# Kernel tuning notes

Hardware: AMD Instinct MI355X
Metric: run time of the kernel (lower is better)

## Reference

```python
import jax, jax.numpy as jnp
import numpy as np

ALPHA = 1.702   # GLU sigmoid scale
LIMIT = 7.0     # clamp limit
K = 2           # experts per token


def setup_inputs() -> dict:
    key = jax.random.key(0)
    ks = jax.random.split(key, 4)
    B, S, H, E, I = 1, 1024, 1024, 8, 1024
    return {
        "hidden_states": jax.random.normal(ks[0], (B, S, H), jnp.float32),
        "router_weight": jax.random.normal(ks[1], (E, H), jnp.float32),
        "router_bias": jnp.zeros((E,), jnp.float32),
        "gate_up_proj": jax.random.normal(ks[2], (E, H, 2 * I), jnp.float32) * 0.02,
        "gate_up_bias": jnp.zeros((E, 2 * I), jnp.float32),
        "down_proj": jax.random.normal(ks[3], (E, I, H), jnp.float32) * 0.02,
        "down_bias": jnp.zeros((E, H), jnp.float32),
    }


def reference(hidden_states, router_weight, router_bias, gate_up_proj,
              gate_up_bias, down_proj, down_bias):
    B, S, H = hidden_states.shape
    E = router_weight.shape[0]
    I = down_proj.shape[1]
    T = B * S

    flat = hidden_states.reshape(T, H)

    # Router: softmax over experts, top-K selection (weights NOT renormalized).
    logits = flat @ router_weight.T + router_bias               # [T, E]
    scores = jax.nn.softmax(logits, axis=-1)
    topk_vals, topk_idx = jax.lax.top_k(scores, K)              # [T, K]

    # Dense per-token expert weight matrix (equivalent of dispatch metadata +
    # combine * topk_weights in the tt pipeline); top-k indices are unique.
    w = jnp.zeros((T, E), scores.dtype).at[
        jnp.arange(T)[:, None], topk_idx].set(topk_vals)        # [T, E]

    # Expert MLP with clamped GLU (gpt-oss style).
    gu = jnp.einsum('th,ehf->tef', flat, gate_up_proj) + gate_up_bias  # [T,E,2I]
    gate = jnp.minimum(gu[..., :I], LIMIT)
    up = jnp.clip(gu[..., I:], -LIMIT, LIMIT)
    glu = gate * jax.nn.sigmoid(gate * ALPHA)
    act = (up + 1.0) * glu                                       # [T, E, I]

    down = jnp.einsum('tei,eih->teh', act, down_proj) + down_bias  # [T, E, H]

    # Weighted combine over selected experts.
    out = jnp.einsum('teh,te->th', down, w)
    return out.reshape(B, S, H)
```

## Files before the change

### kernel.cpp

```cpp
#include <hip/hip_runtime.h>
#include <hip/hip_bf16.h>


typedef unsigned short u16;
typedef __attribute__((ext_vector_type(8))) __bf16 bf16x8;
typedef __attribute__((ext_vector_type(4))) float f32x4;

#define T_TOK 1024
#define H_DIM 1024
#define E_NUM 8
#define I_DIM 1024
#define ALPHA 1.702f
#define LIMIT 7.0f
#define LSTR 72

__device__ __forceinline__ u16 f2bf(float f) {
    unsigned u = __builtin_bit_cast(unsigned, f);
    u = (u + 0x7FFFu + ((u >> 16) & 1u)) >> 16;
    return (u16)u;
}

__device__ __forceinline__ unsigned pk2(float lo, float hi) {
#if defined(__has_builtin) && __has_builtin(__builtin_amdgcn_cvt_pk_bf16_f32)
    typedef __attribute__((ext_vector_type(2))) __bf16 bf16x2_t;
    bf16x2_t v = __builtin_amdgcn_cvt_pk_bf16_f32(lo, hi);
    return __builtin_bit_cast(unsigned, v);
#else
    return (unsigned)f2bf(lo) | ((unsigned)f2bf(hi) << 16);
#endif
}

__device__ __forceinline__ f32x4 mfma16(bf16x8 a, bf16x8 b, f32x4 c) {
    return __builtin_amdgcn_mfma_f32_16x16x32_bf16(a, b, c, 0, 0, 0);
}

__device__ __forceinline__ void expert_range(const int* counts, int e,
                                             int& cnt, int& abase) {
    int a = 0, c = 0;
#pragma unroll
    for (int i = 0; i < E_NUM; ++i) {
        int v = counts[i];
        if (i < e) a += v;
        if (i == e) c = v;
    }
    cnt = c; abase = a;
}

__global__ void k_zero(int* counts) {
    if (threadIdx.x < E_NUM) counts[threadIdx.x] = 0;
}

__global__ __launch_bounds__(256) void k_router(
    const float* __restrict__ x, const float* __restrict__ rw,
    const float* __restrict__ rb, const float* __restrict__ db,
    int* __restrict__ counts, int* __restrict__ tok_list,
    float* __restrict__ w_list, u16* __restrict__ xb,
    float* __restrict__ out)
{
    const int t = blockIdx.x;
    const int tid = threadIdx.x;
    const float4 xv = *(const float4*)(x + (size_t)t * H_DIM + tid * 4);

    *(uint2*)(xb + (size_t)t * H_DIM + tid * 4) =
        make_uint2(pk2(xv.x, xv.y), pk2(xv.z, xv.w));

    float p[E_NUM];
#pragma unroll
    for (int e = 0; e < E_NUM; ++e) {
        const float4 wv = *(const float4*)(rw + e * H_DIM + tid * 4);
        p[e] = xv.x * wv.x + xv.y * wv.y + xv.z * wv.z + xv.w * wv.w;
    }
#pragma unroll
    for (int off = 32; off; off >>= 1) {
#pragma unroll
        for (int e = 0; e < E_NUM; ++e) p[e] += __shfl_down(p[e], off, 64);
    }
    __shared__ float red[4][E_NUM];
    __shared__ int se[2];
    __shared__ float sw[2];
    const int lane = tid & 63, wvid = tid >> 6;
    if (lane == 0) {
#pragma unroll
        for (int e = 0; e < E_NUM; ++e) red[wvid][e] = p[e];
    }
    __syncthreads();
    if (tid == 0) {
        float lg[E_NUM];
#pragma unroll
        for (int e = 0; e < E_NUM; ++e)
            lg[e] = red[0][e] + red[1][e] + red[2][e] + red[3][e] + rb[e];
        float m1 = -1e30f, m2 = -1e30f; int i1 = 0, i2 = 0;
#pragma unroll
        for (int e = 0; e < E_NUM; ++e) {
            float l = lg[e];
            if (l > m1) { m2 = m1; i2 = i1; m1 = l; i1 = e; }
            else if (l > m2) { m2 = l; i2 = e; }
        }
        float s = 0.f;
#pragma unroll
        for (int e = 0; e < E_NUM; ++e) s += __expf(lg[e] - m1);
        const float w0 = 1.0f / s;
        const float w1 = __expf(m2 - m1) / s;
        int slot0 = atomicAdd(&counts[i1], 1);
        tok_list[i1 * T_TOK + slot0] = t;
        w_list[i1 * T_TOK + slot0] = w0;
        int slot1 = atomicAdd(&counts[i2], 1);
        tok_list[i2 * T_TOK + slot1] = t;
        w_list[i2 * T_TOK + slot1] = w1;
        se[0] = i1; se[1] = i2; sw[0] = w0; sw[1] = w1;
    }
    __syncthreads();
    const int e0 = se[0], e1 = se[1];
    const float w0 = sw[0], w1 = sw[1];
    const int c = tid * 4;
    float4 d0 = *(const float4*)(db + e0 * H_DIM + c);
    float4 d1 = *(const float4*)(db + e1 * H_DIM + c);
    float4 o;
    o.x = w0 * d0.x + w1 * d1.x;
    o.y = w0 * d0.y + w1 * d1.y;
    o.z = w0 * d0.z + w1 * d1.z;
    o.w = w0 * d0.w + w1 * d1.w;
    *(float4*)(out + (size_t)t * H_DIM + c) = o;
}

__global__ __launch_bounds__(256) void k_gateup(
    const float* __restrict__ gup, const float* __restrict__ gub,
    const int* __restrict__ counts, const int* __restrict__ tok_list,
    const u16* __restrict__ xb, u16* __restrict__ act)
{
    const int e = blockIdx.z;
    int cnt, abase;
    expert_range(counts, e, cnt, abase);
    const int m0 = blockIdx.y * 64;
    if (m0 >= cnt) return;
    const int n0 = blockIdx.x * 32;
    const int tid = threadIdx.x;

    __shared__ __align__(16) u16 As[64 * LSTR];
    __shared__ __align__(16) u16 Bs[64 * LSTR];
    unsigned* Bs32 = (unsigned*)Bs;

    const int arow_i = tid >> 2, akq = (tid & 3) * 16;
    const int aslot = m0 + arow_i;
    const int atok = (aslot < cnt) ? tok_list[e * T_TOK + aslot] : 0;
    const u16* asrc = xb + (size_t)atok * H_DIM + akq;
    u16* adst = &As[arow_i * LSTR + akq];

    const int kp = tid >> 3, q = tid & 7;
    const float* bgate = gup + ((size_t)e << 21) + n0 + q * 4;

    const int lane = tid & 63, wv = tid >> 6;
    const int fm = lane & 15, kg = lane >> 4;

    f32x4 accg[2], accu[2];
#pragma unroll
    for (int nt = 0; nt < 2; ++nt) {
        accg[nt] = (f32x4){0.f, 0.f, 0.f, 0.f};
        accu[nt] = (f32x4){0.f, 0.f, 0.f, 0.f};
    }

#define GU_LOAD(A0, A1, G0, G1, U0, U1, KB)                                    \
    {                                                                          \
        const u16* ap_ = asrc + (KB);                                          \
        A0 = *(const uint4*)(ap_);                                             \
        A1 = *(const uint4*)(ap_ + 8);                                         \
        const float* gp_ = bgate + (size_t)((KB) + 2 * kp) * 2048;             \
        G0 = *(const float4*)(gp_);                                            \
        G1 = *(const float4*)(gp_ + 2048);                                     \
        U0 = *(const float4*)(gp_ + 1024);                                     \
        U1 = *(const float4*)(gp_ + 3072);                                     \
    }
#define GU_STORE(A0, A1, G0, G1, U0, U1)                                       \
    {                                                                          \
        *(uint4*)adst       = A0;                                              \
        *(uint4*)(adst + 8) = A1;                                              \
        const float* g0_ = (const float*)&G0; const float* g1_ = (const float*)&G1; \
        const float* u0_ = (const float*)&U0; const float* u1_ = (const float*)&U1; \
        _Pragma("unroll")                                                      \
        for (int j = 0; j < 4; ++j) {                                          \
            Bs32[(q * 4 + j) * 36 + kp]        = pk2(g0_[j], g1_[j]);          \
            Bs32[(32 + q * 4 + j) * 36 + kp]   = pk2(u0_[j], u1_[j]);          \
        }                                                                      \
    }
#define GU_MFMA()                                                              \
    {                                                                          \
        _Pragma("unroll")                                                      \
        for (int sub = 0; sub < 2; ++sub) {                                    \
            bf16x8 af = *(const bf16x8*)&As[(wv * 16 + fm) * LSTR + sub * 32 + kg * 8]; \
            _Pragma("unroll")                                                  \
            for (int nt = 0; nt < 2; ++nt) {                                   \
                bf16x8 bg = *(const bf16x8*)&Bs[(nt * 16 + fm) * LSTR + sub * 32 + kg * 8]; \
                bf16x8 bu = *(const bf16x8*)&Bs[(32 + nt * 16 + fm) * LSTR + sub * 32 + kg * 8]; \
                accg[nt] = mfma16(af, bg, accg[nt]);                           \
                accu[nt] = mfma16(af, bu, accu[nt]);                           \
            }                                                                  \
        }                                                                      \
    }

    uint4 a0s0, a1s0, a0s1, a1s1;
    float4 g0s0, g1s0, u0s0, u1s0, g0s1, g1s1, u0s1, u1s1;
    GU_LOAD(a0s0, a1s0, g0s0, g1s0, u0s0, u1s0, 0);
    GU_LOAD(a0s1, a1s1, g0s1, g1s1, u0s1, u1s1, 64);

    for (int kb = 0; kb < H_DIM; kb += 128) {
        __syncthreads();
        GU_STORE(a0s0, a1s0, g0s0, g1s0, u0s0, u1s0);
        if (kb + 128 < H_DIM) GU_LOAD(a0s0, a1s0, g0s0, g1s0, u0s0, u1s0, kb + 128);
        __syncthreads();
        GU_MFMA();

        __syncthreads();
        GU_STORE(a0s1, a1s1, g0s1, g1s1, u0s1, u1s1);
        if (kb + 192 < H_DIM) GU_LOAD(a0s1, a1s1, g0s1, g1s1, u0s1, u1s1, kb + 192);
        __syncthreads();
        GU_MFMA();
    }
#undef GU_LOAD
#undef GU_STORE
#undef GU_MFMA

#pragma unroll
    for (int r = 0; r < 4; ++r) {
        int rowb = wv * 16 + kg * 4 + r;
        int slot = m0 + rowb;
        if (slot >= cnt) continue;
        size_t arow_o = (size_t)(abase + slot) * I_DIM;
#pragma unroll
        for (int nt = 0; nt < 2; ++nt) {
            int cn = n0 + nt * 16 + fm;
            float g = accg[nt][r] + gub[e * 2048 + cn];
            float u = accu[nt][r] + gub[e * 2048 + 1024 + cn];
            g = fminf(g, LIMIT);
            u = fminf(fmaxf(u, -LIMIT), LIMIT);
            float glu = g / (1.f + __expf(-ALPHA * g));
            act[arow_o + cn] = f2bf((u + 1.f) * glu);
        }
    }
}

__global__ __launch_bounds__(256) void k_down(
    const float* __restrict__ dp,
    const int* __restrict__ counts, const int* __restrict__ tok_list,
    const float* __restrict__ w_list,
    const u16* __restrict__ act, float* __restrict__ out)
{
    const int e = blockIdx.z & 7, ks = blockIdx.z >> 3;
    int cnt, abase;
    expert_range(counts, e, cnt, abase);
    const int m0 = blockIdx.y * 64;
    if (m0 >= cnt) return;
    const int n0 = blockIdx.x * 64;
    const int tid = threadIdx.x;

    __shared__ __align__(16) u16 As[64 * LSTR];
    __shared__ __align__(16) u16 Bs[64 * LSTR];
    unsigned* Bs32 = (unsigned*)Bs;

    const int arow_i = tid >> 2, akq = (tid & 3) * 16;
    const u16* asrc = act + (size_t)(abase + m0 + arow_i) * I_DIM + ks * 512 + akq;
    u16* adst = &As[arow_i * LSTR + akq];

    const int kp = tid >> 3, q = tid & 7;
    const float* bsrc = dp + ((size_t)e << 20) + (size_t)(ks * 512) * 1024 + n0 + q * 4;

    const int lane = tid & 63, wv = tid >> 6;
    const int fm = lane & 15, kg = lane >> 4;

    f32x4 acc[4];
#pragma unroll
    for (int nt = 0; nt < 4; ++nt) acc[nt] = (f32x4){0.f, 0.f, 0.f, 0.f};

#define DN_LOAD(A0, A1, B00, B01, B10, B11, KB)                                \
    {                                                                          \
        const u16* ap_ = asrc + (KB);                                          \
        A0 = *(const uint4*)(ap_);                                             \
        A1 = *(const uint4*)(ap_ + 8);                                         \
        const float* bp_ = bsrc + (size_t)((KB) + 2 * kp) * 1024;              \
        B00 = *(const float4*)(bp_);                                           \
        B01 = *(const float4*)(bp_ + 1024);                                    \
        B10 = *(const float4*)(bp_ + 32);                                      \
        B11 = *(const float4*)(bp_ + 1056);                                    \
    }
#define DN_STORE(A0, A1, B00, B01, B10, B11)                                   \
    {                                                                          \
        *(uint4*)adst       = A0;                                              \
        *(uint4*)(adst + 8) = A1;                                              \
        const float* b00_ = (const float*)&B00; const float* b01_ = (const float*)&B01; \
        const float* b10_ = (const float*)&B10; const float* b11_ = (const float*)&B11; \
        _Pragma("unroll")                                                      \
        for (int j = 0; j < 4; ++j) {                                          \
            Bs32[(q * 4 + j) * 36 + kp]      = pk2(b00_[j], b01_[j]);          \
            Bs32[(32 + q * 4 + j) * 36 + kp] = pk2(b10_[j], b11_[j]);          \
        }                                                                      \
    }
#define DN_MFMA()                                                              \
    {                                                                          \
        _Pragma("unroll")                                                      \
        for (int sub = 0; sub < 2; ++sub) {                                    \
            bf16x8 af = *(const bf16x8*)&As[(wv * 16 + fm) * LSTR + sub * 32 + kg * 8]; \
            _Pragma("unroll")                                                  \
            for (int nt = 0; nt < 4; ++nt) {                                   \
                bf16x8 b = *(const bf16x8*)&Bs[(nt * 16 + fm) * LSTR + sub * 32 + kg * 8]; \
                acc[nt] = mfma16(af, b, acc[nt]);                              \
            }                                                                  \
        }                                                                      \
    }

    uint4 a0s0, a1s0, a0s1, a1s1;
    float4 b00s0, b01s0, b10s0, b11s0, b00s1, b01s1, b10s1, b11s1;
    DN_LOAD(a0s0, a1s0, b00s0, b01s0, b10s0, b11s0, 0);
    DN_LOAD(a0s1, a1s1, b00s1, b01s1, b10s1, b11s1, 64);

    for (int kb = 0; kb < 512; kb += 128) {
        __syncthreads();
        DN_STORE(a0s0, a1s0, b00s0, b01s0, b10s0, b11s0);
        if (kb + 128 < 512) DN_LOAD(a0s0, a1s0, b00s0, b01s0, b10s0, b11s0, kb + 128);
        __syncthreads();
        DN_MFMA();

        __syncthreads();
        DN_STORE(a0s1, a1s1, b00s1, b01s1, b10s1, b11s1);
        if (kb + 192 < 512) DN_LOAD(a0s1, a1s1, b00s1, b01s1, b10s1, b11s1, kb + 192);
        __syncthreads();
        DN_MFMA();
    }
#undef DN_LOAD
#undef DN_STORE
#undef DN_MFMA

#pragma unroll
    for (int r = 0; r < 4; ++r) {
        int rowb = wv * 16 + kg * 4 + r;
        int slot = m0 + rowb;
        if (slot >= cnt) continue;
        float wgt = w_list[e * T_TOK + slot];
        int tok = tok_list[e * T_TOK + slot];
        float* orow = out + (size_t)tok * H_DIM + n0;
#pragma unroll
        for (int nt = 0; nt < 4; ++nt)
            atomicAdd(orow + nt * 16 + fm, acc[nt][r] * wgt);
    }
}

extern "C" void kernel_launch(void* const* d_in, const int* in_sizes, int n_in,
                              void* d_out, int out_size, void* d_ws, size_t ws_size,
                              hipStream_t stream) {
    const float* x   = (const float*)d_in[0];
    const float* rw  = (const float*)d_in[1];
    const float* rb  = (const float*)d_in[2];
    const float* gup = (const float*)d_in[3];
    const float* gub = (const float*)d_in[4];
    const float* dp  = (const float*)d_in[5];
    const float* db  = (const float*)d_in[6];
    float* out = (float*)d_out;

    char* ws = (char*)d_ws;
    int*   counts   = (int*)(ws);
    int*   tok_list = (int*)(ws + 64);
    float* w_list   = (float*)(ws + 64 + 32768);
    u16*   xb       = (u16*)(ws + 65600);
    u16*   act      = (u16*)(ws + 65600 + 2097152);

    k_zero<<<1, 64, 0, stream>>>(counts);
    k_router<<<T_TOK, 256, 0, stream>>>(x, rw, rb, db, counts, tok_list, w_list,
                                        xb, out);
    k_gateup<<<dim3(32, 16, 8), 256, 0, stream>>>(gup, gub, counts, tok_list,
                                                  xb, act);
    k_down<<<dim3(16, 16, 16), 256, 0, stream>>>(dp, counts, tok_list, w_list,
                                                 act, out);
}
```

Before: 210.8 us.

## Double-buffer LDS tiles in gate-up and down expert GEMMs

Both expert GEMM kernels now keep two shared-memory A/B tile buffers. The next tile is written into one buffer while MFMAs read the other, which halves the barriers per k-step from four to two. Launch bounds also request four blocks per CU, trading register budget for occupancy. Shared memory per block doubles, which may limit residency or force register spills.

```diff
diff --git a/kernel.cpp b/kernel.cpp
--- a/kernel.cpp
+++ b/kernel.cpp
@@ -123,7 +123,7 @@
     *(float4*)(out + (size_t)t * H_DIM + c) = o;
 }
 
-__global__ __launch_bounds__(256) void k_gateup(
+__global__ __launch_bounds__(256, 4) void k_gateup(
     const float* __restrict__ gup, const float* __restrict__ gub,
     const int* __restrict__ counts, const int* __restrict__ tok_list,
     const u16* __restrict__ xb, u16* __restrict__ act)
@@ -136,15 +136,19 @@
     const int n0 = blockIdx.x * 32;
     const int tid = threadIdx.x;
 
-    __shared__ __align__(16) u16 As[64 * LSTR];
-    __shared__ __align__(16) u16 Bs[64 * LSTR];
-    unsigned* Bs32 = (unsigned*)Bs;
+    __shared__ __align__(16) u16 As0[64 * LSTR];
+    __shared__ __align__(16) u16 Bs0[64 * LSTR];
+    __shared__ __align__(16) u16 As1[64 * LSTR];
+    __shared__ __align__(16) u16 Bs1[64 * LSTR];
+    unsigned* B32_0 = (unsigned*)Bs0;
+    unsigned* B32_1 = (unsigned*)Bs1;
 
     const int arow_i = tid >> 2, akq = (tid & 3) * 16;
     const int aslot = m0 + arow_i;
     const int atok = (aslot < cnt) ? tok_list[e * T_TOK + aslot] : 0;
     const u16* asrc = xb + (size_t)atok * H_DIM + akq;
-    u16* adst = &As[arow_i * LSTR + akq];
+    u16* adst0 = &As0[arow_i * LSTR + akq];
+    u16* adst1 = &As1[arow_i * LSTR + akq];
 
     const int kp = tid >> 3, q = tid & 7;
     const float* bgate = gup + ((size_t)e << 21) + n0 + q * 4;
@@ -170,27 +174,27 @@
         U0 = *(const float4*)(gp_ + 1024);                                     \
         U1 = *(const float4*)(gp_ + 3072);                                     \
     }
-#define GU_STORE(A0, A1, G0, G1, U0, U1)                                       \
-    {                                                                          \
-        *(uint4*)adst       = A0;                                              \
-        *(uint4*)(adst + 8) = A1;                                              \
+#define GU_STORE(AD, B32, A0, A1, G0, G1, U0, U1)                              \
+    {                                                                          \
+        *(uint4*)(AD)       = A0;                                              \
+        *(uint4*)((AD) + 8) = A1;                                              \
         const float* g0_ = (const float*)&G0; const float* g1_ = (const float*)&G1; \
         const float* u0_ = (const float*)&U0; const float* u1_ = (const float*)&U1; \
         _Pragma("unroll")                                                      \
         for (int j = 0; j < 4; ++j) {                                          \
-            Bs32[(q * 4 + j) * 36 + kp]        = pk2(g0_[j], g1_[j]);          \
-            Bs32[(32 + q * 4 + j) * 36 + kp]   = pk2(u0_[j], u1_[j]);          \
+            B32[(q * 4 + j) * 36 + kp]        = pk2(g0_[j], g1_[j]);           \
+            B32[(32 + q * 4 + j) * 36 + kp]   = pk2(u0_[j], u1_[j]);           \
         }                                                                      \
     }
-#define GU_MFMA()                                                              \
+#define GU_MFMA(AS, BS)                                                        \
     {                                                                          \
         _Pragma("unroll")                                                      \
         for (int sub = 0; sub < 2; ++sub) {                                    \
-            bf16x8 af = *(const bf16x8*)&As[(wv * 16 + fm) * LSTR + sub * 32 + kg * 8]; \
+            bf16x8 af = *(const bf16x8*)&AS[(wv * 16 + fm) * LSTR + sub * 32 + kg * 8]; \
             _Pragma("unroll")                                                  \
             for (int nt = 0; nt < 2; ++nt) {                                   \
-                bf16x8 bg = *(const bf16x8*)&Bs[(nt * 16 + fm) * LSTR + sub * 32 + kg * 8]; \
-                bf16x8 bu = *(const bf16x8*)&Bs[(32 + nt * 16 + fm) * LSTR + sub * 32 + kg * 8]; \
+                bf16x8 bg = *(const bf16x8*)&BS[(nt * 16 + fm) * LSTR + sub * 32 + kg * 8]; \
+                bf16x8 bu = *(const bf16x8*)&BS[(32 + nt * 16 + fm) * LSTR + sub * 32 + kg * 8]; \
                 accg[nt] = mfma16(af, bg, accg[nt]);                           \
                 accu[nt] = mfma16(af, bu, accu[nt]);                           \
             }                                                                  \
@@ -201,19 +205,23 @@
     float4 g0s0, g1s0, u0s0, u1s0, g0s1, g1s1, u0s1, u1s1;
     GU_LOAD(a0s0, a1s0, g0s0, g1s0, u0s0, u1s0, 0);
     GU_LOAD(a0s1, a1s1, g0s1, g1s1, u0s1, u1s1, 64);
+    GU_STORE(adst0, B32_0, a0s0, a1s0, g0s0, g1s0, u0s0, u1s0);
+    GU_LOAD(a0s0, a1s0, g0s0, g1s0, u0s0, u1s0, 128);
+    __syncthreads();
 
     for (int kb = 0; kb < H_DIM; kb += 128) {
+        GU_STORE(adst1, B32_1, a0s1, a1s1, g0s1, g1s1, u0s1, u1s1);
+        if (kb + 192 < H_DIM)
+            GU_LOAD(a0s1, a1s1, g0s1, g1s1, u0s1, u1s1, kb + 192);
+        GU_MFMA(As0, Bs0);
         __syncthreads();
-        GU_STORE(a0s0, a1s0, g0s0, g1s0, u0s0, u1s0);
-        if (kb + 128 < H_DIM) GU_LOAD(a0s0, a1s0, g0s0, g1s0, u0s0, u1s0, kb + 128);
+        if (kb + 128 < H_DIM) {
+            GU_STORE(adst0, B32_0, a0s0, a1s0, g0s0, g1s0, u0s0, u1s0);
+            if (kb + 256 < H_DIM)
+                GU_LOAD(a0s0, a1s0, g0s0, g1s0, u0s0, u1s0, kb + 256);
+        }
+        GU_MFMA(As1, Bs1);
         __syncthreads();
-        GU_MFMA();
-
-        __syncthreads();
-        GU_STORE(a0s1, a1s1, g0s1, g1s1, u0s1, u1s1);
-        if (kb + 192 < H_DIM) GU_LOAD(a0s1, a1s1, g0s1, g1s1, u0s1, u1s1, kb + 192);
-        __syncthreads();
-        GU_MFMA();
     }
 #undef GU_LOAD
 #undef GU_STORE
@@ -238,7 +246,7 @@
     }
 }
 
-__global__ __launch_bounds__(256) void k_down(
+__global__ __launch_bounds__(256, 4) void k_down(
     const float* __restrict__ dp,
     const int* __restrict__ counts, const int* __restrict__ tok_list,
     const float* __restrict__ w_list,
@@ -252,13 +260,17 @@
     const int n0 = blockIdx.x * 64;
     const int tid = threadIdx.x;
 
-    __shared__ __align__(16) u16 As[64 * LSTR];
-    __shared__ __align__(16) u16 Bs[64 * LSTR];
-    unsigned* Bs32 = (unsigned*)Bs;
+    __shared__ __align__(16) u16 As0[64 * LSTR];
+    __shared__ __align__(16) u16 Bs0[64 * LSTR];
+    __shared__ __align__(16) u16 As1[64 * LSTR];
+    __shared__ __align__(16) u16 Bs1[64 * LSTR];
+    unsigned* B32_0 = (unsigned*)Bs0;
+    unsigned* B32_1 = (unsigned*)Bs1;
 
     const int arow_i = tid >> 2, akq = (tid & 3) * 16;
     const u16* asrc = act + (size_t)(abase + m0 + arow_i) * I_DIM + ks * 512 + akq;
-    u16* adst = &As[arow_i * LSTR + akq];
+    u16* adst0 = &As0[arow_i * LSTR + akq];
+    u16* adst1 = &As1[arow_i * LSTR + akq];
 
     const int kp = tid >> 3, q = tid & 7;
     const float* bsrc = dp + ((size_t)e << 20) + (size_t)(ks * 512) * 1024 + n0 + q * 4;
@@ -281,26 +293,26 @@
         B10 = *(const float4*)(bp_ + 32);                                      \
         B11 = *(const float4*)(bp_ + 1056);                                    \
     }
-#define DN_STORE(A0, A1, B00, B01, B10, B11)                                   \
-    {                                                                          \
-        *(uint4*)adst       = A0;                                              \
-        *(uint4*)(adst + 8) = A1;                                              \
+#define DN_STORE(AD, B32, A0, A1, B00, B01, B10, B11)                          \
+    {                                                                          \
+        *(uint4*)(AD)       = A0;                                              \
+        *(uint4*)((AD) + 8) = A1;                                              \
         const float* b00_ = (const float*)&B00; const float* b01_ = (const float*)&B01; \
         const float* b10_ = (const float*)&B10; const float* b11_ = (const float*)&B11; \
         _Pragma("unroll")                                                      \
         for (int j = 0; j < 4; ++j) {                                          \
-            Bs32[(q * 4 + j) * 36 + kp]      = pk2(b00_[j], b01_[j]);          \
-            Bs32[(32 + q * 4 + j) * 36 + kp] = pk2(b10_[j], b11_[j]);          \
+            B32[(q * 4 + j) * 36 + kp]      = pk2(b00_[j], b01_[j]);           \
+            B32[(32 + q * 4 + j) * 36 + kp] = pk2(b10_[j], b11_[j]);           \
         }                                                                      \
     }
-#define DN_MFMA()                                                              \
+#define DN_MFMA(AS, BS)                                                        \
     {                                                                          \
         _Pragma("unroll")                                                      \
         for (int sub = 0; sub < 2; ++sub) {                                    \
-            bf16x8 af = *(const bf16x8*)&As[(wv * 16 + fm) * LSTR + sub * 32 + kg * 8]; \
+            bf16x8 af = *(const bf16x8*)&AS[(wv * 16 + fm) * LSTR + sub * 32 + kg * 8]; \
             _Pragma("unroll")                                                  \
             for (int nt = 0; nt < 4; ++nt) {                                   \
-                bf16x8 b = *(const bf16x8*)&Bs[(nt * 16 + fm) * LSTR + sub * 32 + kg * 8]; \
+                bf16x8 b = *(const bf16x8*)&BS[(nt * 16 + fm) * LSTR + sub * 32 + kg * 8]; \
                 acc[nt] = mfma16(af, b, acc[nt]);                              \
             }                                                                  \
         }                                                                      \
@@ -310,19 +322,23 @@
     float4 b00s0, b01s0, b10s0, b11s0, b00s1, b01s1, b10s1, b11s1;
     DN_LOAD(a0s0, a1s0, b00s0, b01s0, b10s0, b11s0, 0);
     DN_LOAD(a0s1, a1s1, b00s1, b01s1, b10s1, b11s1, 64);
+    DN_STORE(adst0, B32_0, a0s0, a1s0, b00s0, b01s0, b10s0, b11s0);
+    DN_LOAD(a0s0, a1s0, b00s0, b01s0, b10s0, b11s0, 128);
+    __syncthreads();
 
     for (int kb = 0; kb < 512; kb += 128) {
+        DN_STORE(adst1, B32_1, a0s1, a1s1, b00s1, b01s1, b10s1, b11s1);
+        if (kb + 192 < 512)
+            DN_LOAD(a0s1, a1s1, b00s1, b01s1, b10s1, b11s1, kb + 192);
+        DN_MFMA(As0, Bs0);
         __syncthreads();
-        DN_STORE(a0s0, a1s0, b00s0, b01s0, b10s0, b11s0);
-        if (kb + 128 < 512) DN_LOAD(a0s0, a1s0, b00s0, b01s0, b10s0, b11s0, kb + 128);
+        if (kb + 128 < 512) {
+            DN_STORE(adst0, B32_0, a0s0, a1s0, b00s0, b01s0, b10s0, b11s0);
+            if (kb + 256 < 512)
+                DN_LOAD(a0s0, a1s0, b00s0, b01s0, b10s0, b11s0, kb + 256);
+        }
+        DN_MFMA(As1, Bs1);
         __syncthreads();
-        DN_MFMA();
-
-        __syncthreads();
-        DN_STORE(a0s1, a1s1, b00s1, b01s1, b10s1, b11s1);
-        if (kb + 192 < 512) DN_LOAD(a0s1, a1s1, b00s1, b01s1, b10s1, b11s1, kb + 192);
-        __syncthreads();
-        DN_MFMA();
     }
 #undef DN_LOAD
 #undef DN_STORE
```

Measured after the change: 213.8 us. No clear change (+1.4%).
